# Kernel tuning notes

Hardware: AMD Instinct MI355X
Metric: run time of the kernel (lower is better)

The kernel has to match this reference:

```python
import jax, jax.numpy as jnp
import numpy as np
import math

B, S, D = 4, 2048, 1024
H, DH = 16, 64  # num_heads, head dim (hardcoded 64 in module)


def setup_inputs() -> dict:
    key = jax.random.key(0)
    ks = jax.random.split(key, 5)
    scale = 0.02
    return {
        "x": jax.random.normal(ks[0], (B, S, D), dtype=jnp.float32),
        "W_Q": jax.random.normal(ks[1], (D, H * DH), dtype=jnp.float32) * scale,
        "W_K": jax.random.normal(ks[2], (D, H * DH), dtype=jnp.float32) * scale,
        "W_V": jax.random.normal(ks[3], (D, H * DH), dtype=jnp.float32) * scale,
        "W_O": jax.random.normal(ks[4], (H * DH, D), dtype=jnp.float32) * scale,
        "ln_gamma": jnp.ones((D,), dtype=jnp.float32),
        "ln_beta": jnp.zeros((D,), dtype=jnp.float32),
    }


def reference(x, W_Q, W_K, W_V, W_O, ln_gamma, ln_beta):
    # QKV projections (bias=False Linear: x @ W)
    q = (x @ W_Q).reshape(B, S, H, DH).transpose(0, 2, 1, 3)  # [B,H,S,DH]
    k = (x @ W_K).reshape(B, S, H, DH).transpose(0, 2, 1, 3)
    v = (x @ W_V).reshape(B, S, H, DH).transpose(0, 2, 1, 3)

    # scaled scores with causal mask (upper triangle, diag=1 -> -1e7)
    scores = jnp.einsum("bhsd,bhtd->bhst", q, k) / math.sqrt(DH)  # [B,H,S,S]
    causal = jnp.triu(jnp.ones((S, S), dtype=bool), k=1)
    scores = jnp.where(causal, jnp.float32(-1e7), scores)
    attn = jax.nn.softmax(scores, axis=-1)
    ctx = jnp.einsum("bhst,bhtd->bhsd", attn, v)  # [B,H,S,DH]

    # merge heads, output proj, residual, LayerNorm
    out = ctx.transpose(0, 2, 1, 3).reshape(B, S, H * DH) @ W_O + x
    mu = jnp.mean(out, axis=-1, keepdims=True)
    var = jnp.mean((out - mu) ** 2, axis=-1, keepdims=True)
    out = (out - mu) * jax.lax.rsqrt(var + 1e-5) * ln_gamma + ln_beta
    return out
```

## Files before the change

kernel.cpp:

```cpp
#include <hip/hip_runtime.h>
#include <hip/hip_bf16.h>
#include <cstdint>
#include <cstddef>

#define S_ 2048
#define D_ 1024
#define H_ 16
#define DH_ 64
#define M_ 8192

using bf16 = __bf16;
using bf16x4 = __attribute__((ext_vector_type(4))) __bf16;
using bf16x8 = __attribute__((ext_vector_type(8))) __bf16;
using f32x4 = __attribute__((ext_vector_type(4))) float;
using s16x4 = __attribute__((ext_vector_type(4))) short;

__device__ __forceinline__ void g2lds16(const bf16* g, bf16* l) {
  __builtin_amdgcn_global_load_lds(
      (const __attribute__((address_space(1))) void*)g,
      (__attribute__((address_space(3))) void*)l, 16, 0, 0);
}

__device__ __forceinline__ f32x4 mfma16(bf16x4 a, bf16x4 b, f32x4 c) {
#if __has_builtin(__builtin_amdgcn_mfma_f32_16x16x16_bf16)
  return __builtin_amdgcn_mfma_f32_16x16x16_bf16(a, b, c, 0, 0, 0);
#elif __has_builtin(__builtin_amdgcn_mfma_f32_16x16x16bf16_1k)
  return __builtin_amdgcn_mfma_f32_16x16x16bf16_1k(
      __builtin_bit_cast(s16x4, a), __builtin_bit_cast(s16x4, b), c, 0, 0, 0);
#else
  f32x4 d;
  asm("v_mfma_f32_16x16x16_bf16 %0, %1, %2, %3"
      : "=v"(d)
      : "v"(a), "v"(b), "v"(c));
  return d;
#endif
}

__global__ __launch_bounds__(256) void cvt_all_kernel(
    const float* __restrict__ x, const float* __restrict__ w0,
    const float* __restrict__ w1, const float* __restrict__ w2,
    const float* __restrict__ w3, bf16* __restrict__ xb,
    bf16* __restrict__ o0, bf16* __restrict__ o1, bf16* __restrict__ o2,
    bf16* __restrict__ o3) {
  __shared__ float tile[32][33];
  int bx = blockIdx.x;
  int tid = threadIdx.x;
  if (bx < 4096) {
    size_t i = ((size_t)bx * 256 + tid) * 8;
    float4 a = *(const float4*)(x + i);
    float4 b = *(const float4*)(x + i + 4);
    bf16x8 o;
    o[0] = (bf16)a.x; o[1] = (bf16)a.y; o[2] = (bf16)a.z; o[3] = (bf16)a.w;
    o[4] = (bf16)b.x; o[5] = (bf16)b.y; o[6] = (bf16)b.z; o[7] = (bf16)b.w;
    *(bf16x8*)(xb + i) = o;
    return;
  }
  int wb = bx - 4096;
  int wsel = wb >> 10; wb &= 1023;
  const float* W; bf16* O;
  switch (wsel) {
    case 0: W = w0; O = o0; break;
    case 1: W = w1; O = o1; break;
    case 2: W = w2; O = o2; break;
    default: W = w3; O = o3; break;
  }
  int n0 = (wb & 31) * 32;
  int k0 = (wb >> 5) * 32;
#pragma unroll
  for (int i = 0; i < 4; ++i) {
    int e = tid + i * 256; int rr = e >> 5, cc = e & 31;
    tile[rr][cc] = W[(size_t)(k0 + rr) * 1024 + n0 + cc];
  }
  __syncthreads();
#pragma unroll
  for (int i = 0; i < 4; ++i) {
    int e = tid + i * 256; int rr = e >> 5, cc = e & 31;
    O[(size_t)(n0 + rr) * 1024 + k0 + cc] = (bf16)tile[cc][rr];
  }
}

template <int MODE>
__global__ __launch_bounds__(512, 2) void gemm_kernel(
    const bf16* __restrict__ A,
    const bf16* __restrict__ Bt0, const bf16* __restrict__ Bt1,
    const bf16* __restrict__ Bt2,
    bf16* __restrict__ Qo, bf16* __restrict__ Ko, bf16* __restrict__ Vto,
    const float* __restrict__ xres, float* __restrict__ out) {
  extern __shared__ float4 smem4[];
  bf16* smem = (bf16*)smem4;

  constexpr int NWG = (MODE == 0) ? 768 : 256;
  constexpr int CPX = NWG / 8;
  constexpr int NBN = (MODE == 0) ? 12 : 4;
  const int wg = ((int)blockIdx.x & 7) * CPX + ((int)blockIdx.x >> 3);
  const int bn = wg % NBN, bm = wg / NBN;

  const bf16* Bt;
  int n0full = 0, wsel = 0;
  if constexpr (MODE == 0) {
    wsel = bn >> 2;
    Bt = (wsel == 0) ? Bt0 : (wsel == 1 ? Bt1 : Bt2);
    n0full = (bn & 3) * 256;
  } else {
    Bt = Bt0;
    n0full = bn * 256;
  }

  const int tid = threadIdx.x;
  const int wave = tid >> 6, lane = tid & 63;
  const int quad = lane >> 4, r = lane & 15;
  const int wm = (wave >> 2) * 64, wn = (wave & 3) * 64;

  const int lrow = lane >> 3;
  const int lcol = ((lane & 7) ^ lrow) * 8;
  const int am0 = bm * 128 + wave * 8 + lrow;
  const int am1 = am0 + 64;
  const bf16 *p0, *p1, *p2, *p3, *p4, *p5;
  if constexpr (MODE == 0) {
    p0 = A + (size_t)am0 * 1024 + lcol;
    p1 = A + (size_t)am1 * 1024 + lcol;
  } else {
    p0 = A + (size_t)(am0 >> 11) * (16 * (size_t)S_ * DH_) +
         (size_t)(am0 & 2047) * 64 + lcol;
    p1 = A + (size_t)(am1 >> 11) * (16 * (size_t)S_ * DH_) +
         (size_t)(am1 & 2047) * 64 + lcol;
  }
  const int bnr = n0full + wave * 8 + lrow;
  p2 = Bt + (size_t)bnr * 1024 + lcol;
  p3 = Bt + (size_t)(bnr + 64) * 1024 + lcol;
  p4 = Bt + (size_t)(bnr + 128) * 1024 + lcol;
  p5 = Bt + (size_t)(bnr + 192) * 1024 + lcol;
  constexpr ptrdiff_t dA = (MODE == 0) ? 64 : (ptrdiff_t)S_ * DH_;

  const int oA0 = wave * 512, oA1 = (8 + wave) * 512;
  const int oB0 = 8192 + wave * 512, oB1 = 8192 + (8 + wave) * 512;
  const int oB2 = 8192 + (16 + wave) * 512, oB3 = 8192 + (24 + wave) * 512;

  auto stage = [&](bf16* base) {
    g2lds16(p0, base + oA0); p0 += dA;
    g2lds16(p1, base + oA1); p1 += dA;
    g2lds16(p2, base + oB0); p2 += 64;
    g2lds16(p3, base + oB1); p3 += 64;
    g2lds16(p4, base + oB2); p4 += 64;
    g2lds16(p5, base + oB3); p5 += 64;
  };

  f32x4 acc[4][4];
  const f32x4 zero = {0.f, 0.f, 0.f, 0.f};
#pragma unroll
  for (int i = 0; i < 4; ++i)
#pragma unroll
    for (int j = 0; j < 4; ++j) acc[i][j] = zero;

  const int rw = r & 7;
  const int x0 = (quad ^ rw) * 8;
  const int x1 = ((quad + 4) ^ rw) * 8;
  const int raB = (wm + r) * 64;
  const int rbB = (wn + r) * 64;

  auto phases = [&](const bf16* buf) {
    const bf16* bA = buf;
    const bf16* bB = buf + 8192;
    bf16x8 af[4], bg[4];
#pragma unroll
    for (int i = 0; i < 4; ++i)
      af[i] = *(const bf16x8*)(bA + raB + i * 1024 + x0);
#pragma unroll
    for (int j = 0; j < 4; ++j)
      bg[j] = *(const bf16x8*)(bB + rbB + j * 1024 + x0);
    __builtin_amdgcn_s_setprio(1);
#pragma unroll
    for (int i = 0; i < 4; ++i)
#pragma unroll
      for (int j = 0; j < 4; ++j)
        acc[i][j] = __builtin_amdgcn_mfma_f32_16x16x32_bf16(af[i], bg[j],
                                                            acc[i][j], 0, 0, 0);
    __builtin_amdgcn_s_setprio(0);
    asm volatile("s_barrier" ::: "memory");
#pragma unroll
    for (int i = 0; i < 4; ++i)
      af[i] = *(const bf16x8*)(bA + raB + i * 1024 + x1);
#pragma unroll
    for (int j = 0; j < 4; ++j)
      bg[j] = *(const bf16x8*)(bB + rbB + j * 1024 + x1);
    __builtin_amdgcn_s_setprio(1);
#pragma unroll
    for (int i = 0; i < 4; ++i)
#pragma unroll
      for (int j = 0; j < 4; ++j)
        acc[i][j] = __builtin_amdgcn_mfma_f32_16x16x32_bf16(af[i], bg[j],
                                                            acc[i][j], 0, 0, 0);
    __builtin_amdgcn_s_setprio(0);
  };

  bf16* b0 = smem;
  bf16* b1 = smem + 24576;
  bf16* b2 = smem + 49152;

  stage(b0);
  stage(b1);

#pragma unroll 1
  for (int kt = 0; kt < 15; kt += 3) {
    asm volatile("s_waitcnt vmcnt(6)\n\ts_barrier" ::: "memory");
    stage(b2);
    phases(b0);
    asm volatile("s_waitcnt vmcnt(6)\n\ts_barrier" ::: "memory");
    stage(b0);
    phases(b1);
    asm volatile("s_waitcnt vmcnt(6)\n\ts_barrier" ::: "memory");
    if (kt < 12) stage(b1);
    phases(b2);
  }
  asm volatile("s_waitcnt vmcnt(0)\n\ts_barrier" ::: "memory");
  phases(b0);

  const int mB = bm * 128 + wm + quad * 4;
  if constexpr (MODE == 0) {
    if (wsel < 2) {
      bf16* dst = (wsel == 0) ? Qo : Ko;
#pragma unroll
      for (int i = 0; i < 4; ++i) {
#pragma unroll
        for (int j = 0; j < 4; ++j) {
          int n = n0full + wn + j * 16 + r;
          int h = n >> 6, dh = n & 63;
#pragma unroll
          for (int g = 0; g < 4; ++g) {
            int m = mB + i * 16 + g;
            int b = m >> 11, s = m & 2047;
            dst[((size_t)(b * H_ + h) * S_ + s) * DH_ + dh] =
                (bf16)acc[i][j][g];
          }
        }
      }
    } else {
#pragma unroll
      for (int i = 0; i < 4; ++i) {
        int m = mB + i * 16;
        int b = m >> 11, s = m & 2047;
#pragma unroll
        for (int j = 0; j < 4; ++j) {
          int n = n0full + wn + j * 16 + r;
          int h = n >> 6, dh = n & 63;
          bf16x4 pk;
#pragma unroll
          for (int g = 0; g < 4; ++g) pk[g] = (bf16)acc[i][j][g];
          *(bf16x4*)(Vto + ((size_t)(b * H_ + h) * DH_ + dh) * S_ + s) = pk;
        }
      }
    }
  } else {
#pragma unroll
    for (int i = 0; i < 4; ++i) {
#pragma unroll
      for (int j = 0; j < 4; ++j) {
        int n = bn * 256 + wn + j * 16 + r;
#pragma unroll
        for (int g = 0; g < 4; ++g) {
          int m = mB + i * 16 + g;
          size_t idx = (size_t)m * 1024 + n;
          out[idx] = acc[i][j][g] + xres[idx];
        }
      }
    }
  }
}

__global__ __launch_bounds__(512, 4) void attn_kernel(const bf16* __restrict__ Qb,
                                                      const bf16* __restrict__ Kb,
                                                      const bf16* __restrict__ Vtb,
                                                      bf16* __restrict__ ctx) {
  __shared__ __align__(16) bf16 smK[2][64 * 64];
  __shared__ __align__(16) bf16 smV[2][64 * 64];
  const int bx = blockIdx.x;
  const int bh = bx & 63;
  const int i256 = (bx < 256) ? (7 - (bx >> 6)) : ((bx - 256) >> 6);
  const bf16* Qh = Qb + (size_t)bh * S_ * DH_;
  const bf16* Kh = Kb + (size_t)bh * S_ * DH_;
  const bf16* Vh = Vtb + (size_t)bh * DH_ * S_;
  bf16* Ch = ctx + (size_t)bh * S_ * DH_;
  const int tid = threadIdx.x, wave = tid >> 6, lane = tid & 63;
  const int quad = lane >> 4, r = lane & 15;
  const int r7 = r & 7;
  const int wrow = wave * 8 + (lane >> 3);
  const int gcol = ((lane & 7) ^ (lane >> 3)) * 8;
  const f32x4 zero = {0.f, 0.f, 0.f, 0.f};
  const int xk0 = (quad ^ r7) * 8, xk1 = ((quad + 4) ^ r7) * 8;

  const int q0w = i256 * 256 + wave * 32;
  const int numkt = 4 * i256 + 4;
  const int lastkt = q0w >> 6;

  bf16x8 qf[2][2];
  const float qsc = 0.125f * 1.44269504f;
#pragma unroll
  for (int qg = 0; qg < 2; ++qg)
#pragma unroll
    for (int hh = 0; hh < 2; ++hh) {
      bf16x8 q = *(const bf16x8*)(Qh + (size_t)(q0w + qg * 16 + r) * DH_ +
                                  hh * 32 + quad * 8);
#pragma unroll
      for (int i = 0; i < 8; ++i) q[i] = (bf16)((float)q[i] * qsc);
      qf[qg][hh] = q;
    }

  f32x4 lacc[2] = {zero, zero};
  f32x4 oacc[2][4];
#pragma unroll
  for (int qg = 0; qg < 2; ++qg)
#pragma unroll
    for (int tn = 0; tn < 4; ++tn) oacc[qg][tn] = zero;

  g2lds16(Kh + (size_t)wrow * DH_ + gcol, &smK[0][wave * 512]);
  g2lds16(Vh + (size_t)wrow * S_ + gcol, &smV[0][wave * 512]);
  asm volatile("s_waitcnt vmcnt(0)\n\ts_barrier" ::: "memory");

  for (int kt = 0; kt < numkt; ++kt) {
    const int cur = kt & 1;
    const int kv0 = kt * 64;
    if (kt + 1 < numkt) {
      const int nk = kv0 + 64;
      g2lds16(Kh + (size_t)(nk + wrow) * DH_ + gcol, &smK[1 - cur][wave * 512]);
      g2lds16(Vh + (size_t)wrow * S_ + nk + gcol, &smV[1 - cur][wave * 512]);
    }
    if (kt <= lastkt) {
      const bf16* kb = &smK[cur][0];
      const bf16* vb = &smV[cur][0];

      f32x4 s[2][4];
#pragma unroll
      for (int t = 0; t < 4; ++t) {
        bf16x8 kf0 = *(const bf16x8*)(kb + (t * 16 + r) * 64 + xk0);
        bf16x8 kf1 = *(const bf16x8*)(kb + (t * 16 + r) * 64 + xk1);
#pragma unroll
        for (int qg = 0; qg < 2; ++qg) {
          f32x4 z = __builtin_amdgcn_mfma_f32_16x16x32_bf16(kf0, qf[qg][0],
                                                            zero, 0, 0, 0);
          s[qg][t] = __builtin_amdgcn_mfma_f32_16x16x32_bf16(kf1, qf[qg][1],
                                                             z, 0, 0, 0);
        }
      }
      if (kt == lastkt) {
#pragma unroll
        for (int qg = 0; qg < 2; ++qg) {
          const int q = q0w + qg * 16 + r;
#pragma unroll
          for (int t = 0; t < 4; ++t) {
            const int kv = kv0 + t * 16 + quad * 4;
#pragma unroll
            for (int g = 0; g < 4; ++g)
              if (kv + g > q) s[qg][t][g] = -1e30f;
          }
        }
      }
#pragma unroll
      for (int t = 0; t < 4; ++t) {
        bf16x4 pa[2];
#pragma unroll
        for (int qg = 0; qg < 2; ++qg) {
#pragma unroll
          for (int g = 0; g < 4; ++g)
            s[qg][t][g] = __builtin_amdgcn_exp2f(s[qg][t][g]);
          lacc[qg] += s[qg][t];
          bf16x4 pk;
#pragma unroll
          for (int g = 0; g < 4; ++g) pk[g] = (bf16)s[qg][t][g];
          pa[qg] = pk;
        }
#pragma unroll
        for (int tn = 0; tn < 4; ++tn) {
          bf16x4 vf = *(const bf16x4*)(
              vb + (tn * 16 + r) * 64 +
              ((2 * t + (quad >> 1)) ^ r7) * 8 + (quad & 1) * 4);
          oacc[0][tn] = mfma16(pa[0], vf, oacc[0][tn]);
          oacc[1][tn] = mfma16(pa[1], vf, oacc[1][tn]);
        }
      }
    }
    asm volatile("s_waitcnt vmcnt(0) lgkmcnt(0)\n\ts_barrier" ::: "memory");
  }

#pragma unroll
  for (int qg = 0; qg < 2; ++qg) {
    float rs = (lacc[qg][0] + lacc[qg][1]) + (lacc[qg][2] + lacc[qg][3]);
    rs += __shfl_xor(rs, 16, 64);
    rs += __shfl_xor(rs, 32, 64);
    const float inv = 1.f / rs;
    f32x4 ib;
#pragma unroll
    for (int g = 0; g < 4; ++g) ib[g] = __shfl(inv, quad * 4 + g, 64);
#pragma unroll
    for (int tn = 0; tn < 4; ++tn) {
      f32x4 ov = oacc[qg][tn] * ib;
#pragma unroll
      for (int g = 0; g < 4; ++g)
        Ch[(size_t)(q0w + qg * 16 + quad * 4 + g) * DH_ + tn * 16 + r] =
            (bf16)ov[g];
    }
  }
}

__global__ __launch_bounds__(256) void ln_kernel(float* __restrict__ out,
                                                 const float* __restrict__ gamma,
                                                 const float* __restrict__ beta) {
  __shared__ float red[8];
  size_t row = blockIdx.x;
  float* p = out + row * 1024;
  int tid = threadIdx.x;
  float4 v = ((const float4*)p)[tid];
  float s1 = v.x + v.y + v.z + v.w;
  float s2 = v.x * v.x + v.y * v.y + v.z * v.z + v.w * v.w;
#pragma unroll
  for (int o = 1; o < 64; o <<= 1) {
    s1 += __shfl_xor(s1, o, 64);
    s2 += __shfl_xor(s2, o, 64);
  }
  int wave = tid >> 6, lane = tid & 63;
  if (lane == 0) { red[wave] = s1; red[4 + wave] = s2; }
  __syncthreads();
  s1 = red[0] + red[1] + red[2] + red[3];
  s2 = red[4] + red[5] + red[6] + red[7];
  float mean = s1 * (1.f / 1024.f);
  float var = s2 * (1.f / 1024.f) - mean * mean;
  float rstd = rsqrtf(var + 1e-5f);
  float4 g = ((const float4*)gamma)[tid];
  float4 b = ((const float4*)beta)[tid];
  float4 o;
  o.x = (v.x - mean) * rstd * g.x + b.x;
  o.y = (v.y - mean) * rstd * g.y + b.y;
  o.z = (v.z - mean) * rstd * g.z + b.z;
  o.w = (v.w - mean) * rstd * g.w + b.w;
  ((float4*)p)[tid] = o;
}

extern "C" void kernel_launch(void* const* d_in, const int* in_sizes, int n_in,
                              void* d_out, int out_size, void* d_ws,
                              size_t ws_size, hipStream_t stream) {
  (void)in_sizes; (void)n_in; (void)out_size; (void)ws_size;
  const float* x  = (const float*)d_in[0];
  const float* WQ = (const float*)d_in[1];
  const float* WK = (const float*)d_in[2];
  const float* WV = (const float*)d_in[3];
  const float* WO = (const float*)d_in[4];
  const float* gamma = (const float*)d_in[5];
  const float* beta  = (const float*)d_in[6];
  float* out = (float*)d_out;

  bf16* ws = (bf16*)d_ws;
  const size_t MD = (size_t)M_ * D_;
  const size_t WW = (size_t)D_ * D_;
  bf16* xb   = ws;
  bf16* wqt  = xb + MD;
  bf16* wkt  = wqt + WW;
  bf16* wvt  = wkt + WW;
  bf16* wot  = wvt + WW;
  bf16* Qb   = wot + WW;
  bf16* Kb   = Qb + MD;
  bf16* Vtb  = Kb + MD;
  bf16* ctxb = Vtb + MD;

  constexpr int GEMM_LDS = 3 * 48 * 1024;
  static bool s_attr = false;
  if (!s_attr) {
    s_attr = true;
    (void)hipFuncSetAttribute(reinterpret_cast<const void*>(gemm_kernel<0>),
                              hipFuncAttributeMaxDynamicSharedMemorySize,
                              GEMM_LDS);
    (void)hipFuncSetAttribute(reinterpret_cast<const void*>(gemm_kernel<1>),
                              hipFuncAttributeMaxDynamicSharedMemorySize,
                              GEMM_LDS);
  }

  cvt_all_kernel<<<dim3(8192), dim3(256), 0, stream>>>(
      x, WQ, WK, WV, WO, xb, wqt, wkt, wvt, wot);
  gemm_kernel<0><<<dim3(768), dim3(512), GEMM_LDS, stream>>>(
      xb, wqt, wkt, wvt, Qb, Kb, Vtb, nullptr, nullptr);
  attn_kernel<<<dim3(512), dim3(512), 0, stream>>>(Qb, Kb, Vtb, ctxb);
  gemm_kernel<1><<<dim3(256), dim3(512), GEMM_LDS, stream>>>(
      ctxb, wot, nullptr, nullptr, nullptr, nullptr, nullptr, x, out);
  ln_kernel<<<dim3(8192), dim3(256), 0, stream>>>(out, gamma, beta);
}
```

Measured before the change: 262.4 us.

## Stage two KV tiles per barrier in attention and drop mid-phase GEMM barrier

The attention kernel now loads two 64-wide K/V tiles per pipeline stage into a doubled shared-memory buffer and processes both before the barrier. This halves the number of waitcnt and barrier syncs per key sequence and gives prefetches more time to land. Separately, an s_barrier between the two MFMA phases of the GEMM loop is removed to cut sync overhead. The shared memory per block doubles to 64KB, which may reduce occupancy against the launch bound of 4 blocks. Dropping the GEMM barrier may also change how waves interleave, and is only safe if no shared-memory writes race with those reads.

Result: faster. 254.3 us (-3.1%).

```diff
diff --git a/kernel.cpp b/kernel.cpp
--- a/kernel.cpp
+++ b/kernel.cpp
@@ -176,7 +176,6 @@
         acc[i][j] = __builtin_amdgcn_mfma_f32_16x16x32_bf16(af[i], bg[j],
                                                             acc[i][j], 0, 0, 0);
     __builtin_amdgcn_s_setprio(0);
-    asm volatile("s_barrier" ::: "memory");
 #pragma unroll
     for (int i = 0; i < 4; ++i)
       af[i] = *(const bf16x8*)(bA + raB + i * 1024 + x1);
@@ -271,8 +270,8 @@
                                                       const bf16* __restrict__ Kb,
                                                       const bf16* __restrict__ Vtb,
                                                       bf16* __restrict__ ctx) {
-  __shared__ __align__(16) bf16 smK[2][64 * 64];
-  __shared__ __align__(16) bf16 smV[2][64 * 64];
+  __shared__ __align__(16) bf16 smK[2][2][64 * 64];
+  __shared__ __align__(16) bf16 smV[2][2][64 * 64];
   const int bx = blockIdx.x;
   const int bh = bx & 63;
   const int i256 = (bx < 256) ? (7 - (bx >> 6)) : ((bx - 256) >> 6);
@@ -290,6 +289,7 @@
 
   const int q0w = i256 * 256 + wave * 32;
   const int numkt = 4 * i256 + 4;
+  const int NU = numkt >> 1;
   const int lastkt = q0w >> 6;
 
   bf16x8 qf[2][2];
@@ -312,69 +312,80 @@
 #pragma unroll
     for (int tn = 0; tn < 4; ++tn) oacc[qg][tn] = zero;
 
-  g2lds16(Kh + (size_t)wrow * DH_ + gcol, &smK[0][wave * 512]);
-  g2lds16(Vh + (size_t)wrow * S_ + gcol, &smV[0][wave * 512]);
+  auto STAGE = [&](int u, int b) {
+#pragma unroll
+    for (int sub = 0; sub < 2; ++sub) {
+      const int kt = 2 * u + sub;
+      g2lds16(Kh + (size_t)(kt * 64 + wrow) * DH_ + gcol,
+              &smK[b][sub][wave * 512]);
+      g2lds16(Vh + (size_t)wrow * S_ + kt * 64 + gcol,
+              &smV[b][sub][wave * 512]);
+    }
+  };
+
+  STAGE(0, 0);
   asm volatile("s_waitcnt vmcnt(0)\n\ts_barrier" ::: "memory");
 
-  for (int kt = 0; kt < numkt; ++kt) {
-    const int cur = kt & 1;
-    const int kv0 = kt * 64;
-    if (kt + 1 < numkt) {
-      const int nk = kv0 + 64;
-      g2lds16(Kh + (size_t)(nk + wrow) * DH_ + gcol, &smK[1 - cur][wave * 512]);
-      g2lds16(Vh + (size_t)wrow * S_ + nk + gcol, &smV[1 - cur][wave * 512]);
-    }
-    if (kt <= lastkt) {
-      const bf16* kb = &smK[cur][0];
-      const bf16* vb = &smV[cur][0];
-
-      f32x4 s[2][4];
-#pragma unroll
-      for (int t = 0; t < 4; ++t) {
-        bf16x8 kf0 = *(const bf16x8*)(kb + (t * 16 + r) * 64 + xk0);
-        bf16x8 kf1 = *(const bf16x8*)(kb + (t * 16 + r) * 64 + xk1);
-#pragma unroll
-        for (int qg = 0; qg < 2; ++qg) {
-          f32x4 z = __builtin_amdgcn_mfma_f32_16x16x32_bf16(kf0, qf[qg][0],
-                                                            zero, 0, 0, 0);
-          s[qg][t] = __builtin_amdgcn_mfma_f32_16x16x32_bf16(kf1, qf[qg][1],
-                                                             z, 0, 0, 0);
-        }
-      }
-      if (kt == lastkt) {
-#pragma unroll
-        for (int qg = 0; qg < 2; ++qg) {
-          const int q = q0w + qg * 16 + r;
-#pragma unroll
-          for (int t = 0; t < 4; ++t) {
-            const int kv = kv0 + t * 16 + quad * 4;
+#pragma unroll 1
+  for (int u = 0; u < NU; ++u) {
+    const int b = u & 1;
+    if (u + 1 < NU) STAGE(u + 1, b ^ 1);
+#pragma unroll
+    for (int sub = 0; sub < 2; ++sub) {
+      const int kt = 2 * u + sub;
+      if (kt <= lastkt) {
+        const int kv0 = kt * 64;
+        const bf16* kb = &smK[b][sub][0];
+        const bf16* vb = &smV[b][sub][0];
+
+        f32x4 s[2][4];
+#pragma unroll
+        for (int t = 0; t < 4; ++t) {
+          bf16x8 kf0 = *(const bf16x8*)(kb + (t * 16 + r) * 64 + xk0);
+          bf16x8 kf1 = *(const bf16x8*)(kb + (t * 16 + r) * 64 + xk1);
+#pragma unroll
+          for (int qg = 0; qg < 2; ++qg) {
+            f32x4 z = __builtin_amdgcn_mfma_f32_16x16x32_bf16(kf0, qf[qg][0],
+                                                              zero, 0, 0, 0);
+            s[qg][t] = __builtin_amdgcn_mfma_f32_16x16x32_bf16(kf1, qf[qg][1],
+                                                               z, 0, 0, 0);
+          }
+        }
+        if (kt == lastkt) {
+#pragma unroll
+          for (int qg = 0; qg < 2; ++qg) {
+            const int q = q0w + qg * 16 + r;
+#pragma unroll
+            for (int t = 0; t < 4; ++t) {
+              const int kv = kv0 + t * 16 + quad * 4;
+#pragma unroll
+              for (int g = 0; g < 4; ++g)
+                if (kv + g > q) s[qg][t][g] = -1e30f;
+            }
+          }
+        }
+#pragma unroll
+        for (int t = 0; t < 4; ++t) {
+          bf16x4 pa[2];
+#pragma unroll
+          for (int qg = 0; qg < 2; ++qg) {
 #pragma unroll
             for (int g = 0; g < 4; ++g)
-              if (kv + g > q) s[qg][t][g] = -1e30f;
+              s[qg][t][g] = __builtin_amdgcn_exp2f(s[qg][t][g]);
+            lacc[qg] += s[qg][t];
+            bf16x4 pk;
+#pragma unroll
+            for (int g = 0; g < 4; ++g) pk[g] = (bf16)s[qg][t][g];
+            pa[qg] = pk;
           }
-        }
-      }
-#pragma unroll
-      for (int t = 0; t < 4; ++t) {
-        bf16x4 pa[2];
-#pragma unroll
-        for (int qg = 0; qg < 2; ++qg) {
-#pragma unroll
-          for (int g = 0; g < 4; ++g)
-            s[qg][t][g] = __builtin_amdgcn_exp2f(s[qg][t][g]);
-          lacc[qg] += s[qg][t];
-          bf16x4 pk;
-#pragma unroll
-          for (int g = 0; g < 4; ++g) pk[g] = (bf16)s[qg][t][g];
-          pa[qg] = pk;
-        }
-#pragma unroll
-        for (int tn = 0; tn < 4; ++tn) {
-          bf16x4 vf = *(const bf16x4*)(
-              vb + (tn * 16 + r) * 64 +
-              ((2 * t + (quad >> 1)) ^ r7) * 8 + (quad & 1) * 4);
-          oacc[0][tn] = mfma16(pa[0], vf, oacc[0][tn]);
-          oacc[1][tn] = mfma16(pa[1], vf, oacc[1][tn]);
+#pragma unroll
+          for (int tn = 0; tn < 4; ++tn) {
+            bf16x4 vf = *(const bf16x4*)(
+                vb + (tn * 16 + r) * 64 +
+                ((2 * t + (quad >> 1)) ^ r7) * 8 + (quad & 1) * 4);
+            oacc[0][tn] = mfma16(pa[0], vf, oacc[0][tn]);
+            oacc[1][tn] = mfma16(pa[1], vf, oacc[1][tn]);
+          }
         }
       }
     }
```
